# Optimization experiments

Measured on AMD Instinct MI355X. Metric: run time of the kernel, lower is better.

## Reference

```python
import jax, jax.numpy as jnp
import numpy as np

B, N = 1, 4096
D_IN, D_OUT, H = 256, 256, 8
HD = D_OUT // H
NEG = -9e15


def _xavier(key, shape):
    lim = np.sqrt(6.0 / (shape[0] + shape[1])).astype(np.float32)
    return jax.random.uniform(key, shape, jnp.float32, -lim, lim)


def setup_inputs() -> dict:
    key = jax.random.key(0)
    ks = jax.random.split(key, 8)
    x = jax.random.normal(ks[0], (B, N, D_IN), jnp.float32)
    adj = (jax.random.uniform(ks[1], (B, N, N)) < 0.05).astype(jnp.float32)
    idx = jnp.arange(N)
    adj = adj.at[:, idx, idx].set(1.0)
    Wq = _xavier(ks[2], (D_IN, D_OUT)); bq = jnp.zeros((D_OUT,), jnp.float32)
    Wk = _xavier(ks[3], (D_IN, D_OUT)); bk = jnp.zeros((D_OUT,), jnp.float32)
    Wv = _xavier(ks[4], (D_IN, D_OUT)); bv = jnp.zeros((D_OUT,), jnp.float32)
    Wo = _xavier(ks[5], (D_OUT, D_OUT)); bo = jnp.zeros((D_OUT,), jnp.float32)
    return dict(x=x, adj=adj, Wq=Wq, bq=bq, Wk=Wk, bk=bk, Wv=Wv, bv=bv, Wo=Wo, bo=bo)


def reference(x, adj, Wq, bq, Wk, bk, Wv, bv, Wo, bo):
    b, n, _ = x.shape
    def split_heads(t):  # [B,N,D_OUT] -> [B,H,N,HD]
        return t.reshape(b, n, H, HD).transpose(0, 2, 1, 3)
    q = split_heads(x @ Wq + bq)
    k = split_heads(x @ Wk + bk)
    v = split_heads(x @ Wv + bv)
    scores = jnp.einsum('bhqd,bhkd->bhqk', q, k) / np.float32(np.sqrt(HD))
    scores = jnp.where(adj[:, None, :, :] > 0, scores, jnp.float32(NEG))
    attn = jax.nn.softmax(scores, axis=-1)
    # dropout is identity in eval mode (training=False)
    out = jnp.einsum('bhqk,bhkd->bhqd', attn, v)
    out = out.transpose(0, 2, 1, 3).reshape(b, n, D_OUT)
    return out @ Wo + bo
```

## Files before the change

kernel.cpp:

```cpp
#include <hip/hip_runtime.h>
#include <hip/hip_bf16.h>
#include <stdint.h>

#define NTOK 4096
#define DIM  256
#define NH   8
#define HD   32
#define MAXNNZ 512

typedef __attribute__((ext_vector_type(8))) short short8;
typedef __attribute__((ext_vector_type(4))) float float4v;
typedef unsigned short u16;
typedef unsigned int u32;

__device__ __forceinline__ float bf2f(u16 u) {
    union { u32 u; float f; } c; c.u = ((u32)u) << 16; return c.f;
}
__device__ __forceinline__ u16 f2bf(float f) {
    union { float f; u32 u; } c; c.f = f;
    u32 u = c.u;
    u = u + 0x7FFFu + ((u >> 16) & 1u);
    return (u16)(u >> 16);
}

__global__ void x_to_bf16(const float* __restrict__ x, u16* __restrict__ xb) {
    int i = (blockIdx.x * blockDim.x + threadIdx.x) * 4;
    float4 v = *(const float4*)(x + i);
    ushort4 o;
    o.x = f2bf(v.x); o.y = f2bf(v.y); o.z = f2bf(v.z); o.w = f2bf(v.w);
    *(ushort4*)(xb + i) = o;
}

__global__ void transpose_w(const float* __restrict__ Wq, const float* __restrict__ Wk,
                            const float* __restrict__ Wv, const float* __restrict__ Wo,
                            u16* __restrict__ WT) {
    const float* srcs[4] = {Wq, Wk, Wv, Wo};
    const float* W = srcs[blockIdx.y];
    int o = blockIdx.x, i = threadIdx.x;
    WT[blockIdx.y * 65536 + o * 256 + i] = f2bf(W[i * 256 + o]);
}

__global__ __launch_bounds__(256) void adj_to_list(const float* __restrict__ adj,
                                                   u16* __restrict__ NL,
                                                   u32* __restrict__ NC) {
    __shared__ u32 cnt;
    int row = blockIdx.x, t = threadIdx.x;
    if (t == 0) cnt = 0;
    __syncthreads();
    const float4* rp = (const float4*)(adj + (size_t)row * NTOK);
    u16* lbase = NL + (size_t)row * MAXNNZ;
#pragma unroll
    for (int i = 0; i < 4; ++i) {
        float4 v = rp[i * 256 + t];
        u32 m = 0;
        if (v.x != 0.f) m |= 1u;
        if (v.y != 0.f) m |= 2u;
        if (v.z != 0.f) m |= 4u;
        if (v.w != 0.f) m |= 8u;
        if (m) {
            int p = __popc(m);
            u32 base = atomicAdd(&cnt, (u32)p);
            int col0 = (i * 256 + t) * 4;
            while (m) {
                int j = __builtin_ctz(m);
                m &= m - 1;
                if (base < MAXNNZ) lbase[base] = (u16)(col0 + j);
                ++base;
            }
        }
    }
    __syncthreads();
    if (t == 0) NC[row] = (cnt < MAXNNZ) ? cnt : MAXNNZ;
}

__global__ __launch_bounds__(64) void qkv_gemm(
    const u16* __restrict__ xb,
    const u16* __restrict__ WT,
    const float* __restrict__ bq, const float* __restrict__ bk, const float* __restrict__ bv,
    u16* __restrict__ Q, u16* __restrict__ K, u16* __restrict__ V) {
    int lane = threadIdx.x, quad = lane >> 4, l16 = lane & 15;
    int mtile = blockIdx.x, ntile = blockIdx.y, mat = blockIdx.z;
    const float* bias = (mat == 0) ? bq : (mat == 1) ? bk : bv;
    const u16* arow = xb + (size_t)(mtile * 16 + l16) * DIM + quad * 8;
    const u16* brow = WT + (size_t)mat * 65536 + (size_t)(ntile * 16 + l16) * DIM + quad * 8;
    float4v acc = {0.f, 0.f, 0.f, 0.f};
#pragma unroll
    for (int k0 = 0; k0 < DIM; k0 += 32) {
        short8 af = *(const short8*)(arow + k0);
        short8 bf = *(const short8*)(brow + k0);
        acc = __builtin_amdgcn_mfma_f32_16x16x32_bf16(af, bf, acc, 0, 0, 0);
    }
    int n = ntile * 16 + l16;
    float bb = bias[n];
    const float sc = (mat == 0) ? 0.25503635559913516f : 1.0f;
    u16* dst = (mat == 0) ? Q : (mat == 1) ? K : V;
#pragma unroll
    for (int r = 0; r < 4; ++r) {
        int m = mtile * 16 + quad * 4 + r;
        dst[(size_t)m * DIM + n] = f2bf((acc[r] + bb) * sc);
    }
}

__global__ __launch_bounds__(256, 4) void sparse_attn(
    const u16* __restrict__ Q, const u16* __restrict__ K, const u16* __restrict__ V,
    const u16* __restrict__ NL, const u32* __restrict__ NC,
    u16* __restrict__ AO) {
    int row = blockIdx.x * 4 + (threadIdx.x >> 6);
    int lane = threadIdx.x & 63;
    int l4 = lane * 4;

    ushort4 qu = *(const ushort4*)(Q + (size_t)row * DIM + l4);
    float q0 = bf2f(qu.x), q1 = bf2f(qu.y), q2 = bf2f(qu.z), q3 = bf2f(qu.w);
    float O0 = 0.f, O1 = 0.f, O2 = 0.f, O3 = 0.f, lsum = 0.f;

    int nnz = (int)NC[row];
    const u16* lst = NL + (size_t)row * MAXNNZ;

#define NBR_BODY(kk, vv)                                                          \
    {                                                                             \
        float s = q0 * bf2f(kk.x) + q1 * bf2f(kk.y)                               \
                + q2 * bf2f(kk.z) + q3 * bf2f(kk.w);                              \
        s += __shfl_xor(s, 1, 64);                                                \
        s += __shfl_xor(s, 2, 64);                                                \
        s += __shfl_xor(s, 4, 64);                                                \
        float e = __builtin_amdgcn_exp2f(s);                                      \
        lsum += e;                                                                \
        O0 += e * bf2f(vv.x); O1 += e * bf2f(vv.y);                               \
        O2 += e * bf2f(vv.z); O3 += e * bf2f(vv.w);                               \
    }

    int j = 0;
    for (; j + 8 <= nnz; j += 8) {
        ushort4 i03 = *(const ushort4*)(lst + j);
        ushort4 i47 = *(const ushort4*)(lst + j + 4);
        ushort4 kk[8], vv[8];
        kk[0] = *(const ushort4*)(K + (size_t)i03.x * DIM + l4);
        kk[1] = *(const ushort4*)(K + (size_t)i03.y * DIM + l4);
        kk[2] = *(const ushort4*)(K + (size_t)i03.z * DIM + l4);
        kk[3] = *(const ushort4*)(K + (size_t)i03.w * DIM + l4);
        kk[4] = *(const ushort4*)(K + (size_t)i47.x * DIM + l4);
        kk[5] = *(const ushort4*)(K + (size_t)i47.y * DIM + l4);
        kk[6] = *(const ushort4*)(K + (size_t)i47.z * DIM + l4);
        kk[7] = *(const ushort4*)(K + (size_t)i47.w * DIM + l4);
        vv[0] = *(const ushort4*)(V + (size_t)i03.x * DIM + l4);
        vv[1] = *(const ushort4*)(V + (size_t)i03.y * DIM + l4);
        vv[2] = *(const ushort4*)(V + (size_t)i03.z * DIM + l4);
        vv[3] = *(const ushort4*)(V + (size_t)i03.w * DIM + l4);
        vv[4] = *(const ushort4*)(V + (size_t)i47.x * DIM + l4);
        vv[5] = *(const ushort4*)(V + (size_t)i47.y * DIM + l4);
        vv[6] = *(const ushort4*)(V + (size_t)i47.z * DIM + l4);
        vv[7] = *(const ushort4*)(V + (size_t)i47.w * DIM + l4);
#pragma unroll
        for (int t = 0; t < 8; ++t) NBR_BODY(kk[t], vv[t])
    }
    for (; j + 4 <= nnz; j += 4) {
        ushort4 i03 = *(const ushort4*)(lst + j);
        ushort4 k0 = *(const ushort4*)(K + (size_t)i03.x * DIM + l4);
        ushort4 k1 = *(const ushort4*)(K + (size_t)i03.y * DIM + l4);
        ushort4 k2 = *(const ushort4*)(K + (size_t)i03.z * DIM + l4);
        ushort4 k3 = *(const ushort4*)(K + (size_t)i03.w * DIM + l4);
        ushort4 v0 = *(const ushort4*)(V + (size_t)i03.x * DIM + l4);
        ushort4 v1 = *(const ushort4*)(V + (size_t)i03.y * DIM + l4);
        ushort4 v2 = *(const ushort4*)(V + (size_t)i03.z * DIM + l4);
        ushort4 v3 = *(const ushort4*)(V + (size_t)i03.w * DIM + l4);
        NBR_BODY(k0, v0)
        NBR_BODY(k1, v1)
        NBR_BODY(k2, v2)
        NBR_BODY(k3, v3)
    }
    for (; j < nnz; ++j) {
        int i0 = lst[j];
        ushort4 k0 = *(const ushort4*)(K + (size_t)i0 * DIM + l4);
        ushort4 v0 = *(const ushort4*)(V + (size_t)i0 * DIM + l4);
        NBR_BODY(k0, v0)
    }
#undef NBR_BODY

    float inv = 1.0f / lsum;
    ushort4 o;
    o.x = f2bf(O0 * inv); o.y = f2bf(O1 * inv);
    o.z = f2bf(O2 * inv); o.w = f2bf(O3 * inv);
    *(ushort4*)(AO + (size_t)row * DIM + l4) = o;
}

__global__ __launch_bounds__(64) void out_gemm(
    const u16* __restrict__ AO, const u16* __restrict__ WTo, const float* __restrict__ bo,
    float* __restrict__ out) {
    int lane = threadIdx.x, quad = lane >> 4, l16 = lane & 15;
    int mtile = blockIdx.x, ntile = blockIdx.y;
    const u16* arow = AO + (size_t)(mtile * 16 + l16) * DIM + quad * 8;
    const u16* brow = WTo + (size_t)(ntile * 16 + l16) * DIM + quad * 8;
    float4v acc = {0.f, 0.f, 0.f, 0.f};
#pragma unroll
    for (int k0 = 0; k0 < DIM; k0 += 32) {
        short8 af = *(const short8*)(arow + k0);
        short8 bf = *(const short8*)(brow + k0);
        acc = __builtin_amdgcn_mfma_f32_16x16x32_bf16(af, bf, acc, 0, 0, 0);
    }
    int n = ntile * 16 + l16;
    float bb = bo[n];
#pragma unroll
    for (int r = 0; r < 4; ++r)
        out[(size_t)(mtile * 16 + quad * 4 + r) * DIM + n] = acc[r] + bb;
}

extern "C" void kernel_launch(void* const* d_in, const int* in_sizes, int n_in,
                              void* d_out, int out_size, void* d_ws, size_t ws_size,
                              hipStream_t stream) {
    const float* x   = (const float*)d_in[0];
    const float* adj = (const float*)d_in[1];
    const float* Wq  = (const float*)d_in[2];
    const float* bq  = (const float*)d_in[3];
    const float* Wk  = (const float*)d_in[4];
    const float* bk  = (const float*)d_in[5];
    const float* Wv  = (const float*)d_in[6];
    const float* bv  = (const float*)d_in[7];
    const float* Wo  = (const float*)d_in[8];
    const float* bo  = (const float*)d_in[9];

    char* ws = (char*)d_ws;
    const size_t MB = 1u << 20;
    u16* Q   = (u16*)(ws);
    u16* K   = (u16*)(ws + 2 * MB);
    u16* V   = (u16*)(ws + 4 * MB);
    u16* AO  = (u16*)(ws + 6 * MB);
    u16* WT  = (u16*)(ws + 8 * MB);
    u16* XB  = (u16*)(ws + 8 * MB + 512 * 1024);
    u16* NL  = (u16*)(ws + 11 * MB);
    u32* NC  = (u32*)(ws + 15 * MB);

    x_to_bf16<<<dim3(1024), 256, 0, stream>>>(x, XB);
    transpose_w<<<dim3(256, 4), 256, 0, stream>>>(Wq, Wk, Wv, Wo, WT);
    adj_to_list<<<dim3(4096), 256, 0, stream>>>(adj, NL, NC);
    qkv_gemm<<<dim3(256, 16, 3), 64, 0, stream>>>(XB, WT, bq, bk, bv, Q, K, V);
    sparse_attn<<<dim3(1024), 256, 0, stream>>>(Q, K, V, NL, NC, AO);
    out_gemm<<<dim3(256, 16), 64, 0, stream>>>(AO, WT + 3 * 65536, bo, (float*)d_out);
}
```

Baseline: 217.0 us.

## Remap sparse attention lanes to head-by-neighbor split with full-head dot products

Rewrites the sparse attention kernel so each lane owns one head and one of eight neighbor slots. Every lane loads the full 32-element K and V head slices with 16-byte loads and computes the dot product locally, which removes the per-neighbor shuffle reduction. It also prefetches the next neighbor index inside the loop. The costs are a 32-float accumulator and a 32-float query in registers per lane, which raises register pressure, plus a final cross-lane reduction of all 32 outputs and the normaliser.

```diff
diff --git a/kernel.cpp b/kernel.cpp
--- a/kernel.cpp
+++ b/kernel.cpp
@@ -21,6 +21,12 @@
     u32 u = c.u;
     u = u + 0x7FFFu + ((u >> 16) & 1u);
     return (u16)(u >> 16);
+}
+__device__ __forceinline__ float blo(u32 c) {
+    union { u32 u; float f; } x; x.u = c << 16; return x.f;
+}
+__device__ __forceinline__ float bhi(u32 c) {
+    union { u32 u; float f; } x; x.u = c & 0xFFFF0000u; return x.f;
 }
 
 __global__ void x_to_bf16(const float* __restrict__ x, u16* __restrict__ xb) {
@@ -101,86 +107,92 @@
     }
 }
 
+#define UNPK8(C, B) do { \
+    q[B+0]=blo(C.x); q[B+1]=bhi(C.x); q[B+2]=blo(C.y); q[B+3]=bhi(C.y); \
+    q[B+4]=blo(C.z); q[B+5]=bhi(C.z); q[B+6]=blo(C.w); q[B+7]=bhi(C.w); } while(0)
+
+#define DOT8(C, A, B) do { \
+    A = fmaf(blo(C.x), q[B+0], A); A = fmaf(bhi(C.x), q[B+1], A); \
+    A = fmaf(blo(C.y), q[B+2], A); A = fmaf(bhi(C.y), q[B+3], A); \
+    A = fmaf(blo(C.z), q[B+4], A); A = fmaf(bhi(C.z), q[B+5], A); \
+    A = fmaf(blo(C.w), q[B+6], A); A = fmaf(bhi(C.w), q[B+7], A); } while(0)
+
+#define PV8(C, B) do { \
+    O[B+0]=fmaf(e, blo(C.x), O[B+0]); O[B+1]=fmaf(e, bhi(C.x), O[B+1]); \
+    O[B+2]=fmaf(e, blo(C.y), O[B+2]); O[B+3]=fmaf(e, bhi(C.y), O[B+3]); \
+    O[B+4]=fmaf(e, blo(C.z), O[B+4]); O[B+5]=fmaf(e, bhi(C.z), O[B+5]); \
+    O[B+6]=fmaf(e, blo(C.w), O[B+6]); O[B+7]=fmaf(e, bhi(C.w), O[B+7]); } while(0)
+
 __global__ __launch_bounds__(256, 4) void sparse_attn(
     const u16* __restrict__ Q, const u16* __restrict__ K, const u16* __restrict__ V,
     const u16* __restrict__ NL, const u32* __restrict__ NC,
     u16* __restrict__ AO) {
     int row = blockIdx.x * 4 + (threadIdx.x >> 6);
     int lane = threadIdx.x & 63;
-    int l4 = lane * 4;
-
-    ushort4 qu = *(const ushort4*)(Q + (size_t)row * DIM + l4);
-    float q0 = bf2f(qu.x), q1 = bf2f(qu.y), q2 = bf2f(qu.z), q3 = bf2f(qu.w);
-    float O0 = 0.f, O1 = 0.f, O2 = 0.f, O3 = 0.f, lsum = 0.f;
+    int h = lane & 7;
+    int s = lane >> 3;
+
+    const uint4* qp = (const uint4*)(Q + (size_t)row * DIM + h * HD);
+    uint4 qq0 = qp[0], qq1 = qp[1], qq2 = qp[2], qq3 = qp[3];
+    float q[32];
+    UNPK8(qq0, 0); UNPK8(qq1, 8); UNPK8(qq2, 16); UNPK8(qq3, 24);
+
+    float O[32];
+#pragma unroll
+    for (int i = 0; i < 32; ++i) O[i] = 0.f;
+    float lsum = 0.f;
 
     int nnz = (int)NC[row];
     const u16* lst = NL + (size_t)row * MAXNNZ;
-
-#define NBR_BODY(kk, vv)                                                          \
-    {                                                                             \
-        float s = q0 * bf2f(kk.x) + q1 * bf2f(kk.y)                               \
-                + q2 * bf2f(kk.z) + q3 * bf2f(kk.w);                              \
-        s += __shfl_xor(s, 1, 64);                                                \
-        s += __shfl_xor(s, 2, 64);                                                \
-        s += __shfl_xor(s, 4, 64);                                                \
-        float e = __builtin_amdgcn_exp2f(s);                                      \
-        lsum += e;                                                                \
-        O0 += e * bf2f(vv.x); O1 += e * bf2f(vv.y);                               \
-        O2 += e * bf2f(vv.z); O3 += e * bf2f(vv.w);                               \
-    }
-
-    int j = 0;
-    for (; j + 8 <= nnz; j += 8) {
-        ushort4 i03 = *(const ushort4*)(lst + j);
-        ushort4 i47 = *(const ushort4*)(lst + j + 4);
-        ushort4 kk[8], vv[8];
-        kk[0] = *(const ushort4*)(K + (size_t)i03.x * DIM + l4);
-        kk[1] = *(const ushort4*)(K + (size_t)i03.y * DIM + l4);
-        kk[2] = *(const ushort4*)(K + (size_t)i03.z * DIM + l4);
-        kk[3] = *(const ushort4*)(K + (size_t)i03.w * DIM + l4);
-        kk[4] = *(const ushort4*)(K + (size_t)i47.x * DIM + l4);
-        kk[5] = *(const ushort4*)(K + (size_t)i47.y * DIM + l4);
-        kk[6] = *(const ushort4*)(K + (size_t)i47.z * DIM + l4);
-        kk[7] = *(const ushort4*)(K + (size_t)i47.w * DIM + l4);
-        vv[0] = *(const ushort4*)(V + (size_t)i03.x * DIM + l4);
-        vv[1] = *(const ushort4*)(V + (size_t)i03.y * DIM + l4);
-        vv[2] = *(const ushort4*)(V + (size_t)i03.z * DIM + l4);
-        vv[3] = *(const ushort4*)(V + (size_t)i03.w * DIM + l4);
-        vv[4] = *(const ushort4*)(V + (size_t)i47.x * DIM + l4);
-        vv[5] = *(const ushort4*)(V + (size_t)i47.y * DIM + l4);
-        vv[6] = *(const ushort4*)(V + (size_t)i47.z * DIM + l4);
-        vv[7] = *(const ushort4*)(V + (size_t)i47.w * DIM + l4);
-#pragma unroll
-        for (int t = 0; t < 8; ++t) NBR_BODY(kk[t], vv[t])
-    }
-    for (; j + 4 <= nnz; j += 4) {
-        ushort4 i03 = *(const ushort4*)(lst + j);
-        ushort4 k0 = *(const ushort4*)(K + (size_t)i03.x * DIM + l4);
-        ushort4 k1 = *(const ushort4*)(K + (size_t)i03.y * DIM + l4);
-        ushort4 k2 = *(const ushort4*)(K + (size_t)i03.z * DIM + l4);
-        ushort4 k3 = *(const ushort4*)(K + (size_t)i03.w * DIM + l4);
-        ushort4 v0 = *(const ushort4*)(V + (size_t)i03.x * DIM + l4);
-        ushort4 v1 = *(const ushort4*)(V + (size_t)i03.y * DIM + l4);
-        ushort4 v2 = *(const ushort4*)(V + (size_t)i03.z * DIM + l4);
-        ushort4 v3 = *(const ushort4*)(V + (size_t)i03.w * DIM + l4);
-        NBR_BODY(k0, v0)
-        NBR_BODY(k1, v1)
-        NBR_BODY(k2, v2)
-        NBR_BODY(k3, v3)
-    }
-    for (; j < nnz; ++j) {
-        int i0 = lst[j];
-        ushort4 k0 = *(const ushort4*)(K + (size_t)i0 * DIM + l4);
-        ushort4 v0 = *(const ushort4*)(V + (size_t)i0 * DIM + l4);
-        NBR_BODY(k0, v0)
-    }
-#undef NBR_BODY
-
-    float inv = 1.0f / lsum;
-    ushort4 o;
-    o.x = f2bf(O0 * inv); o.y = f2bf(O1 * inv);
-    o.z = f2bf(O2 * inv); o.w = f2bf(O3 * inv);
-    *(ushort4*)(AO + (size_t)row * DIM + l4) = o;
+    const u16* Kh = K + h * HD;
+    const u16* Vh = V + h * HD;
+
+    int jj = (s < nnz) ? s : (nnz - 1);
+    int idx = lst[jj];
+    for (int j0 = 0; j0 < nnz; j0 += 8) {
+        bool valid = (j0 + s) < nnz;
+        const uint4* kp = (const uint4*)(Kh + (size_t)idx * DIM);
+        const uint4* vp = (const uint4*)(Vh + (size_t)idx * DIM);
+        uint4 k0 = kp[0], k1 = kp[1], k2 = kp[2], k3 = kp[3];
+        uint4 v0 = vp[0], v1 = vp[1], v2 = vp[2], v3 = vp[3];
+        int jn = j0 + 8 + s;
+        jn = (jn < nnz) ? jn : (nnz - 1);
+        idx = lst[jn];
+
+        float a0 = 0.f, a1 = 0.f, a2 = 0.f, a3 = 0.f;
+        DOT8(k0, a0, 0); DOT8(k1, a1, 8); DOT8(k2, a2, 16); DOT8(k3, a3, 24);
+        float sd = (a0 + a1) + (a2 + a3);
+        float e = __builtin_amdgcn_exp2f(sd);
+        e = valid ? e : 0.f;
+        lsum += e;
+        PV8(v0, 0); PV8(v1, 8); PV8(v2, 16); PV8(v3, 24);
+    }
+
+#pragma unroll
+    for (int i = 0; i < 32; ++i) O[i] += __shfl_xor(O[i], 8, 64);
+#pragma unroll
+    for (int i = 0; i < 32; ++i) O[i] += __shfl_xor(O[i], 16, 64);
+#pragma unroll
+    for (int i = 0; i < 32; ++i) O[i] += __shfl_xor(O[i], 32, 64);
+    lsum += __shfl_xor(lsum, 8, 64);
+    lsum += __shfl_xor(lsum, 16, 64);
+    lsum += __shfl_xor(lsum, 32, 64);
+
+    if (s == 0) {
+        float inv = 1.0f / lsum;
+        u32 w[16];
+#pragma unroll
+        for (int i = 0; i < 16; ++i) {
+            u32 lo16 = (u32)f2bf(O[2 * i] * inv);
+            u32 hi16 = (u32)f2bf(O[2 * i + 1] * inv);
+            w[i] = lo16 | (hi16 << 16);
+        }
+        uint4* dst = (uint4*)(AO + (size_t)row * DIM + h * HD);
+        dst[0] = make_uint4(w[0], w[1], w[2], w[3]);
+        dst[1] = make_uint4(w[4], w[5], w[6], w[7]);
+        dst[2] = make_uint4(w[8], w[9], w[10], w[11]);
+        dst[3] = make_uint4(w[12], w[13], w[14], w[15]);
+    }
 }
 
 __global__ __launch_bounds__(64) void out_gemm(
```

Result: faster. 212.0 us (-2.3%).
